# Kernel optimization log

Measured on AMD Instinct MI355X. Metric: run time of the kernel, lower is better.

The kernel has to match this reference:

```python
import jax, jax.numpy as jnp
import numpy as np

D = 2048
N = 65536


def setup_inputs() -> dict:
    key = jax.random.key(0)
    k1, k2, k3, k4, k5 = jax.random.split(key, 5)
    return {
        "embed_word_l": jax.random.normal(k1, (1, D), dtype=jnp.float32),
        "embed_word_r": jax.random.normal(k2, (1, D), dtype=jnp.float32),
        "embed_candidates_l": jax.random.normal(k3, (N, D), dtype=jnp.float32),
        "embed_candidates_r": jax.random.normal(k4, (N, D), dtype=jnp.float32),
        "W_a": jax.random.truncated_normal(k5, -2.0, 2.0, (D, D), dtype=jnp.float32) * 0.5,
        "b_a": jnp.zeros((1, D), dtype=jnp.float32),
    }


def _determine_attention(embed_word, embed_opposite_candidates, W_a, b_a):
    # embed_word: [1, D]; embed_opposite_candidates: [N, D]
    align = jnp.tanh(embed_word @ W_a + b_a)                 # [1, D]
    scores = embed_opposite_candidates @ align.T             # [N, 1]
    attn = jax.nn.softmax(scores, axis=0)                    # softmax over candidates
    return jnp.sum(attn * embed_opposite_candidates, axis=0, keepdims=True)  # [1, D]


def reference(embed_word_l, embed_word_r, embed_candidates_l, embed_candidates_r, W_a, b_a):
    embed_aggre_word_l = _determine_attention(embed_word_l, embed_candidates_r, W_a, b_a)
    embed_aggre_word_r = _determine_attention(embed_word_r, embed_candidates_l, W_a, b_a)
    return (embed_aggre_word_l, embed_aggre_word_r)
```

## Files before the change

kernel.cpp:

```cpp
#include <hip/hip_runtime.h>
#include <math.h>

#define DDIM 2048
#define NCAND 65536
#define KSPLIT 32
#define BATCH 8

__global__ void align_partial(const float* __restrict__ wl,
                              const float* __restrict__ wr,
                              const float* __restrict__ W,
                              float* __restrict__ alignp) {
    const int j  = blockIdx.x * blockDim.x + threadIdx.x;
    const int kc = blockIdx.y;
    const int kchunk = DDIM / KSPLIT;
    const int k0 = kc * kchunk;
    float al = 0.f, ar = 0.f;
    for (int k = k0; k < k0 + kchunk; ++k) {
        float w = W[(size_t)k * DDIM + j];
        al = fmaf(wl[k], w, al);
        ar = fmaf(wr[k], w, ar);
    }
    alignp[(size_t)(0 * KSPLIT + kc) * DDIM + j] = al;
    alignp[(size_t)(1 * KSPLIT + kc) * DDIM + j] = ar;
}

__global__ void align_finish(const float* __restrict__ alignp,
                             const float* __restrict__ b,
                             float* __restrict__ alignv) {
    const int j = blockIdx.x * blockDim.x + threadIdx.x;
    float sl = b[j], sr = b[j];
    for (int kc = 0; kc < KSPLIT; ++kc) {
        sl += alignp[(size_t)(0 * KSPLIT + kc) * DDIM + j];
        sr += alignp[(size_t)(1 * KSPLIT + kc) * DDIM + j];
    }
    alignv[j] = tanhf(sl);
    alignv[DDIM + j] = tanhf(sr);
}

__global__ __launch_bounds__(256) void score_accum(
    const float* __restrict__ cand_l, const float* __restrict__ cand_r,
    const float* __restrict__ alignv,
    float* __restrict__ accP, float* __restrict__ mP, float* __restrict__ sP,
    int B, int rows_per_block)
{
    const int side = blockIdx.y;
    const float* __restrict__ cand  = (side == 0) ? cand_r : cand_l;
    const float* __restrict__ align = alignv + (size_t)side * DDIM;

    const int t    = threadIdx.x;
    const int wave = t >> 6;
    const int lane = t & 63;
    const int c0 = t * 4;
    const int c1 = DDIM / 2 + t * 4;

    const float4 al0 = *(const float4*)(align + c0);
    const float4 al1 = *(const float4*)(align + c1);

    float4 acc0 = {0.f, 0.f, 0.f, 0.f};
    float4 acc1 = {0.f, 0.f, 0.f, 0.f};

    __shared__ float sh_part[BATCH][4];
    __shared__ float sh_w[BATCH];
    __shared__ float sh_alpha;
    __shared__ float sh_m, sh_s;
    if (t == 0) { sh_m = -INFINITY; sh_s = 0.f; }

    const int row0 = blockIdx.x * rows_per_block;
    for (int rb = 0; rb < rows_per_block; rb += BATCH) {
        const float* rp = cand + (size_t)(row0 + rb) * DDIM;
        float4 v0[BATCH], v1[BATCH];
        float part[BATCH];
#pragma unroll
        for (int r = 0; r < BATCH; ++r) {
            v0[r] = *(const float4*)(rp + (size_t)r * DDIM + c0);
            v1[r] = *(const float4*)(rp + (size_t)r * DDIM + c1);
            part[r] = v0[r].x * al0.x + v0[r].y * al0.y + v0[r].z * al0.z + v0[r].w * al0.w
                    + v1[r].x * al1.x + v1[r].y * al1.y + v1[r].z * al1.z + v1[r].w * al1.w;
        }
#pragma unroll
        for (int r = 0; r < BATCH; ++r) {
            float p = part[r];
            for (int off = 32; off > 0; off >>= 1)
                p += __shfl_down(p, off, 64);
            if (lane == 0) sh_part[r][wave] = p;
        }
        __syncthreads();
        if (t == 0) {
            float m_old = sh_m;
            float bm = m_old;
            float sc[BATCH];
#pragma unroll
            for (int r = 0; r < BATCH; ++r) {
                sc[r] = sh_part[r][0] + sh_part[r][1] + sh_part[r][2] + sh_part[r][3];
                bm = fmaxf(bm, sc[r]);
            }
            float alpha = expf(m_old - bm);
            float ssum = 0.f;
#pragma unroll
            for (int r = 0; r < BATCH; ++r) {
                float w = expf(sc[r] - bm);
                sh_w[r] = w;
                ssum += w;
            }
            sh_s = sh_s * alpha + ssum;
            sh_m = bm;
            sh_alpha = alpha;
        }
        __syncthreads();
        const float alpha = sh_alpha;
        acc0.x *= alpha; acc0.y *= alpha; acc0.z *= alpha; acc0.w *= alpha;
        acc1.x *= alpha; acc1.y *= alpha; acc1.z *= alpha; acc1.w *= alpha;
#pragma unroll
        for (int r = 0; r < BATCH; ++r) {
            const float w = sh_w[r];
            acc0.x = fmaf(w, v0[r].x, acc0.x);
            acc0.y = fmaf(w, v0[r].y, acc0.y);
            acc0.z = fmaf(w, v0[r].z, acc0.z);
            acc0.w = fmaf(w, v0[r].w, acc0.w);
            acc1.x = fmaf(w, v1[r].x, acc1.x);
            acc1.y = fmaf(w, v1[r].y, acc1.y);
            acc1.z = fmaf(w, v1[r].z, acc1.z);
            acc1.w = fmaf(w, v1[r].w, acc1.w);
        }
    }
    float* acc = accP + (size_t)(side * B + blockIdx.x) * DDIM;
    *(float4*)(acc + c0) = acc0;
    *(float4*)(acc + c1) = acc1;
    if (t == 0) {
        mP[side * B + blockIdx.x] = sh_m;
        sP[side * B + blockIdx.x] = sh_s;
    }
}

__global__ void combine(const float* __restrict__ accP,
                        const float* __restrict__ mP,
                        const float* __restrict__ sP,
                        float* __restrict__ out, int B)
{
    const int side = blockIdx.y;
    const int j = blockIdx.x * blockDim.x + threadIdx.x;
    const float* m = mP + side * B;
    const float* s = sP + side * B;
    float M = -INFINITY;
    for (int b = 0; b < B; ++b) M = fmaxf(M, m[b]);
    float S = 0.f, num = 0.f;
    for (int b = 0; b < B; ++b) {
        float w = expf(m[b] - M);
        S += w * s[b];
        num = fmaf(w, accP[(size_t)(side * B + b) * DDIM + j], num);
    }
    out[(size_t)side * DDIM + j] = num / S;
}

extern "C" void kernel_launch(void* const* d_in, const int* in_sizes, int n_in,
                              void* d_out, int out_size, void* d_ws, size_t ws_size,
                              hipStream_t stream) {
    const float* wl = (const float*)d_in[0];
    const float* wr = (const float*)d_in[1];
    const float* cl = (const float*)d_in[2];
    const float* cr = (const float*)d_in[3];
    const float* W  = (const float*)d_in[4];
    const float* ba = (const float*)d_in[5];
    float* out = (float*)d_out;
    float* ws  = (float*)d_ws;

    const size_t fixed_f = (size_t)2 * KSPLIT * DDIM + (size_t)2 * DDIM;
    int B = 512;
    while (B > 8) {
        size_t need = (fixed_f + (size_t)4 * B + (size_t)2 * B * DDIM) * sizeof(float);
        if (need <= ws_size) break;
        B >>= 1;
    }
    const int rpb = NCAND / B;

    float* alignp = ws;
    float* alignv = alignp + (size_t)2 * KSPLIT * DDIM;
    float* mP     = alignv + (size_t)2 * DDIM;
    float* sP     = mP + (size_t)2 * B;
    float* accP   = sP + (size_t)2 * B;

    align_partial<<<dim3(DDIM / 256, KSPLIT), 256, 0, stream>>>(wl, wr, W, alignp);
    align_finish<<<dim3(DDIM / 256), 256, 0, stream>>>(alignp, ba, alignv);
    score_accum<<<dim3(B, 2), 256, 0, stream>>>(cl, cr, alignv, accP, mP, sP, B, rpb);
    combine<<<dim3(DDIM / 256, 2), 256, 0, stream>>>(accP, mP, sP, out, B);
}
```

Measured before the change: 1.223 ms.

## Give each wave its own rows with a private online softmax, merge waves at end

The score-and-accumulate kernel now gives each wavefront its own contiguous row range. Each wave runs an independent online softmax in registers, using a butterfly shuffle reduction, instead of syncing the whole block twice per batch of eight rows. The four per-wave partial accumulators are merged through shared memory at the end. This removes block barriers and serial single-thread softmax work from the streaming loop. In exchange there are fewer loads in flight per row (one row at a time), a divergent rescale branch, and 32KB of shared memory per block.

```diff
diff --git a/kernel.cpp b/kernel.cpp
--- a/kernel.cpp
+++ b/kernel.cpp
@@ -4,7 +4,6 @@
 #define DDIM 2048
 #define NCAND 65536
 #define KSPLIT 32
-#define BATCH 8
 
 __global__ void align_partial(const float* __restrict__ wl,
                               const float* __restrict__ wr,
@@ -37,98 +36,106 @@
     alignv[DDIM + j] = tanhf(sr);
 }
 
-__global__ __launch_bounds__(256) void score_accum(
+__global__ __launch_bounds__(256, 4) void score_accum(
     const float* __restrict__ cand_l, const float* __restrict__ cand_r,
     const float* __restrict__ alignv,
     float* __restrict__ accP, float* __restrict__ mP, float* __restrict__ sP,
-    int B, int rows_per_block)
+    int B, int rows_per_wave)
 {
     const int side = blockIdx.y;
     const float* __restrict__ cand  = (side == 0) ? cand_r : cand_l;
     const float* __restrict__ align = alignv + (size_t)side * DDIM;
 
-    const int t    = threadIdx.x;
-    const int wave = t >> 6;
-    const int lane = t & 63;
-    const int c0 = t * 4;
-    const int c1 = DDIM / 2 + t * 4;
+    const int t = threadIdx.x;
+    const int w = t >> 6;
+    const int l = t & 63;
+    const int cbase = l * 4;
 
-    const float4 al0 = *(const float4*)(align + c0);
-    const float4 al1 = *(const float4*)(align + c1);
+    float4 al[8], acc[8];
+#pragma unroll
+    for (int c = 0; c < 8; ++c) {
+        al[c]  = *(const float4*)(align + c * 256 + cbase);
+        acc[c] = make_float4(0.f, 0.f, 0.f, 0.f);
+    }
+    float m = -INFINITY, s = 0.f;
 
-    float4 acc0 = {0.f, 0.f, 0.f, 0.f};
-    float4 acc1 = {0.f, 0.f, 0.f, 0.f};
-
-    __shared__ float sh_part[BATCH][4];
-    __shared__ float sh_w[BATCH];
-    __shared__ float sh_alpha;
-    __shared__ float sh_m, sh_s;
-    if (t == 0) { sh_m = -INFINITY; sh_s = 0.f; }
-
-    const int row0 = blockIdx.x * rows_per_block;
-    for (int rb = 0; rb < rows_per_block; rb += BATCH) {
-        const float* rp = cand + (size_t)(row0 + rb) * DDIM;
-        float4 v0[BATCH], v1[BATCH];
-        float part[BATCH];
+    const int row0 = (blockIdx.x * 4 + w) * rows_per_wave;
+    for (int r = 0; r < rows_per_wave; ++r) {
+        const float* rp = cand + (size_t)(row0 + r) * DDIM;
+        float4 v[8];
 #pragma unroll
-        for (int r = 0; r < BATCH; ++r) {
-            v0[r] = *(const float4*)(rp + (size_t)r * DDIM + c0);
-            v1[r] = *(const float4*)(rp + (size_t)r * DDIM + c1);
-            part[r] = v0[r].x * al0.x + v0[r].y * al0.y + v0[r].z * al0.z + v0[r].w * al0.w
-                    + v1[r].x * al1.x + v1[r].y * al1.y + v1[r].z * al1.z + v1[r].w * al1.w;
+        for (int c = 0; c < 8; ++c)
+            v[c] = *(const float4*)(rp + c * 256 + cbase);
+        float p = 0.f;
+#pragma unroll
+        for (int c = 0; c < 8; ++c) {
+            p = fmaf(v[c].x, al[c].x, p);
+            p = fmaf(v[c].y, al[c].y, p);
+            p = fmaf(v[c].z, al[c].z, p);
+            p = fmaf(v[c].w, al[c].w, p);
         }
 #pragma unroll
-        for (int r = 0; r < BATCH; ++r) {
-            float p = part[r];
-            for (int off = 32; off > 0; off >>= 1)
-                p += __shfl_down(p, off, 64);
-            if (lane == 0) sh_part[r][wave] = p;
-        }
-        __syncthreads();
-        if (t == 0) {
-            float m_old = sh_m;
-            float bm = m_old;
-            float sc[BATCH];
+        for (int off = 32; off > 0; off >>= 1)
+            p += __shfl_xor(p, off, 64);
+        p = __shfl(p, 0, 64);
+
+        if (p > m) {
+            float alpha = expf(m - p);
+            m = p;
+            s = fmaf(s, alpha, 1.f);
 #pragma unroll
-            for (int r = 0; r < BATCH; ++r) {
-                sc[r] = sh_part[r][0] + sh_part[r][1] + sh_part[r][2] + sh_part[r][3];
-                bm = fmaxf(bm, sc[r]);
+            for (int c = 0; c < 8; ++c) {
+                acc[c].x = fmaf(acc[c].x, alpha, v[c].x);
+                acc[c].y = fmaf(acc[c].y, alpha, v[c].y);
+                acc[c].z = fmaf(acc[c].z, alpha, v[c].z);
+                acc[c].w = fmaf(acc[c].w, alpha, v[c].w);
             }
-            float alpha = expf(m_old - bm);
-            float ssum = 0.f;
+        } else {
+            float wgt = expf(p - m);
+            s += wgt;
 #pragma unroll
-            for (int r = 0; r < BATCH; ++r) {
-                float w = expf(sc[r] - bm);
-                sh_w[r] = w;
-                ssum += w;
+            for (int c = 0; c < 8; ++c) {
+                acc[c].x = fmaf(wgt, v[c].x, acc[c].x);
+                acc[c].y = fmaf(wgt, v[c].y, acc[c].y);
+                acc[c].z = fmaf(wgt, v[c].z, acc[c].z);
+                acc[c].w = fmaf(wgt, v[c].w, acc[c].w);
             }
-            sh_s = sh_s * alpha + ssum;
-            sh_m = bm;
-            sh_alpha = alpha;
-        }
-        __syncthreads();
-        const float alpha = sh_alpha;
-        acc0.x *= alpha; acc0.y *= alpha; acc0.z *= alpha; acc0.w *= alpha;
-        acc1.x *= alpha; acc1.y *= alpha; acc1.z *= alpha; acc1.w *= alpha;
-#pragma unroll
-        for (int r = 0; r < BATCH; ++r) {
-            const float w = sh_w[r];
-            acc0.x = fmaf(w, v0[r].x, acc0.x);
-            acc0.y = fmaf(w, v0[r].y, acc0.y);
-            acc0.z = fmaf(w, v0[r].z, acc0.z);
-            acc0.w = fmaf(w, v0[r].w, acc0.w);
-            acc1.x = fmaf(w, v1[r].x, acc1.x);
-            acc1.y = fmaf(w, v1[r].y, acc1.y);
-            acc1.z = fmaf(w, v1[r].z, acc1.z);
-            acc1.w = fmaf(w, v1[r].w, acc1.w);
         }
     }
-    float* acc = accP + (size_t)(side * B + blockIdx.x) * DDIM;
-    *(float4*)(acc + c0) = acc0;
-    *(float4*)(acc + c1) = acc1;
+
+    __shared__ float sh_acc[4][DDIM];
+    __shared__ float sh_m[4], sh_s[4];
+#pragma unroll
+    for (int c = 0; c < 8; ++c)
+        *(float4*)(&sh_acc[w][c * 256 + cbase]) = acc[c];
+    if (l == 0) { sh_m[w] = m; sh_s[w] = s; }
+    __syncthreads();
+
+    const float mB = fmaxf(fmaxf(sh_m[0], sh_m[1]), fmaxf(sh_m[2], sh_m[3]));
+    const float e0 = expf(sh_m[0] - mB);
+    const float e1 = expf(sh_m[1] - mB);
+    const float e2 = expf(sh_m[2] - mB);
+    const float e3 = expf(sh_m[3] - mB);
+    const float sB = e0 * sh_s[0] + e1 * sh_s[1] + e2 * sh_s[2] + e3 * sh_s[3];
+
+    float* accB = accP + (size_t)(side * B + blockIdx.x) * DDIM;
+#pragma unroll
+    for (int half = 0; half < 2; ++half) {
+        const int col = half * 1024 + t * 4;
+        const float4 a0 = *(const float4*)&sh_acc[0][col];
+        const float4 a1 = *(const float4*)&sh_acc[1][col];
+        const float4 a2 = *(const float4*)&sh_acc[2][col];
+        const float4 a3 = *(const float4*)&sh_acc[3][col];
+        float4 o;
+        o.x = e0 * a0.x + e1 * a1.x + e2 * a2.x + e3 * a3.x;
+        o.y = e0 * a0.y + e1 * a1.y + e2 * a2.y + e3 * a3.y;
+        o.z = e0 * a0.z + e1 * a1.z + e2 * a2.z + e3 * a3.z;
+        o.w = e0 * a0.w + e1 * a1.w + e2 * a2.w + e3 * a3.w;
+        *(float4*)(accB + col) = o;
+    }
     if (t == 0) {
-        mP[side * B + blockIdx.x] = sh_m;
-        sP[side * B + blockIdx.x] = sh_s;
+        mP[side * B + blockIdx.x] = mB;
+        sP[side * B + blockIdx.x] = sB;
     }
 }
 
@@ -171,7 +178,7 @@
         if (need <= ws_size) break;
         B >>= 1;
     }
-    const int rpb = NCAND / B;
+    const int rpw = NCAND / (B * 4);
 
     float* alignp = ws;
     float* alignv = alignp + (size_t)2 * KSPLIT * DDIM;
@@ -181,6 +188,6 @@
 
     align_partial<<<dim3(DDIM / 256, KSPLIT), 256, 0, stream>>>(wl, wr, W, alignp);
     align_finish<<<dim3(DDIM / 256), 256, 0, stream>>>(alignp, ba, alignv);
-    score_accum<<<dim3(B, 2), 256, 0, stream>>>(cl, cr, alignv, accP, mP, sP, B, rpb);
+    score_accum<<<dim3(B, 2), 256, 0, stream>>>(cl, cr, alignv, accP, mP, sP, B, rpw);
     combine<<<dim3(DDIM / 256, 2), 256, 0, stream>>>(accP, mP, sP, out, B);
 }
```

New measurement: 1.163 ms. -4.9%, faster.
